# Kernel optimization log

Hardware: AMD Instinct MI355X
Metric: run time of the kernel (lower is better)

The kernel has to match this reference:

```python
import jax, jax.numpy as jnp
import numpy as np

N_HEADS = 16
D_EMBED = 1024
D_HEAD = D_EMBED // N_HEADS
CAUSAL = False


def setup_inputs() -> dict:
    key = jax.random.key(0)
    k1, k2, k3, k4, k5 = jax.random.split(key, 5)
    B, S, D = 4, 2048, D_EMBED
    scale = 1.0 / np.sqrt(D)
    return {
        "x": jax.random.normal(k1, (B, S, D), dtype=jnp.float32),
        "w_in": jax.random.normal(k2, (D, 3 * D), dtype=jnp.float32) * scale,
        "b_in": jax.random.normal(k3, (3 * D,), dtype=jnp.float32) * 0.02,
        "w_out": jax.random.normal(k4, (D, D), dtype=jnp.float32) * scale,
        "b_out": jax.random.normal(k5, (D,), dtype=jnp.float32) * 0.02,
    }


def reference(x, w_in, b_in, w_out, b_out):
    B, S, D = x.shape
    qkv = jnp.einsum("bsd,de->bse", x, w_in) + b_in  # [B,S,3D]
    q, k, v = jnp.split(qkv, 3, axis=-1)
    # split heads -> [B,H,S,Dh]
    def sh(t):
        return t.reshape(B, S, N_HEADS, D_HEAD).transpose(0, 2, 1, 3)
    q, k, v = sh(q), sh(k), sh(v)
    weight = jnp.einsum("bhsd,bhtd->bhst", q, k)  # [B,H,S,S]
    if CAUSAL:
        mask = jnp.triu(jnp.ones((S, S), dtype=bool), k=1)
        weight = jnp.where(mask, -jnp.inf, weight)
    weight = weight / np.sqrt(D_HEAD)
    weight = jax.nn.softmax(weight, axis=-1)
    out = jnp.einsum("bhst,bhtd->bhsd", weight, v)
    out = out.transpose(0, 2, 1, 3).reshape(B, S, D)
    return jnp.einsum("bsd,de->bse", out, w_out) + b_out
```

## Files before the change

### kernel.cpp

```cpp
#include <hip/hip_runtime.h>
#include <hip/hip_bf16.h>

typedef unsigned short u16;
typedef __attribute__((ext_vector_type(8))) short bf16x8;
typedef __attribute__((ext_vector_type(4))) float f32x4;
typedef __attribute__((ext_vector_type(16))) float f32x16;

#define QSCALE 0.180336880f

#define DEV static __device__ __forceinline__

DEV u16 f2bf(float f) {
  union { float f; unsigned u; } v; v.f = f;
  unsigned r = v.u + 0x7fffu + ((v.u >> 16) & 1u);
  return (u16)(r >> 16);
}

DEV unsigned pk2(float a, float b) {
  union { __hip_bfloat162 h; unsigned u; } c;
  c.h = __float22bfloat162_rn(make_float2(a, b));
  return c.u;
}

DEV void gll16(void* lds, const void* g) {
  __builtin_amdgcn_global_load_lds(
      (const __attribute__((address_space(1))) unsigned int*)g,
      (__attribute__((address_space(3))) unsigned int*)lds, 16, 0, 0);
}

__global__ __launch_bounds__(256) void cvt_f32_to_bf16(const float* __restrict__ in,
                                                       u16* __restrict__ out, int n4) {
  int i = blockIdx.x * blockDim.x + threadIdx.x;
  int stride = gridDim.x * blockDim.x;
  for (; i < n4; i += stride) {
    float4 f = ((const float4*)in)[i];
    ushort4 u;
    u.x = f2bf(f.x); u.y = f2bf(f.y); u.z = f2bf(f.z); u.w = f2bf(f.w);
    ((ushort4*)out)[i] = u;
  }
}

__global__ __launch_bounds__(256) void transpose_cvt(const float* __restrict__ W,
                                                     u16* __restrict__ Wt,
                                                     int K, int N, int sn, float sval) {
  __shared__ u16 t[64][65];
  const int k0 = blockIdx.x * 64, n0 = blockIdx.y * 64;
  const int tid = threadIdx.x;
  const int rr = tid >> 4;
  const int cc = (tid & 15) * 4;
  const float scl = (n0 < sn) ? sval : 1.0f;
#pragma unroll
  for (int i = 0; i < 4; ++i) {
    const int row = rr * 4 + i;
    float4 f = *(const float4*)&W[(size_t)(k0 + row) * N + n0 + cc];
    t[row][cc + 0] = f2bf(f.x * scl);
    t[row][cc + 1] = f2bf(f.y * scl);
    t[row][cc + 2] = f2bf(f.z * scl);
    t[row][cc + 3] = f2bf(f.w * scl);
  }
  __syncthreads();
#pragma unroll
  for (int i = 0; i < 4; ++i) {
    const int n = rr * 4 + i;
    ushort4 u;
    u.x = t[cc + 0][n]; u.y = t[cc + 1][n]; u.z = t[cc + 2][n]; u.w = t[cc + 3][n];
    *(ushort4*)&Wt[(size_t)(n0 + n) * K + k0 + cc] = u;
  }
}

__global__ __launch_bounds__(256) void transpose_v(const u16* __restrict__ qkv,
                                                   u16* __restrict__ vT) {
  __shared__ u16 t[64][72];
  const int bh = blockIdx.y;
  const int b = bh >> 4, h = bh & 15;
  const int t0 = blockIdx.x * 64;
  const int tid = threadIdx.x;
  const int row = tid >> 2;
  const int cg = (tid & 3) * 16;
  const size_t src = (size_t)b * 2048 * 3072 + (size_t)(t0 + row) * 3072 + 2048 + h * 64 + cg;
  bf16x8 v0 = *(const bf16x8*)&qkv[src];
  bf16x8 v1 = *(const bf16x8*)&qkv[src + 8];
#pragma unroll
  for (int i = 0; i < 8; ++i) { t[row][cg + i] = (u16)v0[i]; t[row][cg + 8 + i] = (u16)v1[i]; }
  __syncthreads();
  const int d = tid >> 2;
  const int tg = (tid & 3) * 16;
  bf16x8 o0, o1;
#pragma unroll
  for (int i = 0; i < 8; ++i) { o0[i] = (short)t[tg + i][d]; o1[i] = (short)t[tg + 8 + i][d]; }
  u16* dst = &vT[((size_t)bh * 64 + d) * 2048 + t0 + tg];
  *(bf16x8*)dst = o0;
  *(bf16x8*)(dst + 8) = o1;
}

template<bool OUT_BF16>
__global__ __launch_bounds__(256) void gemm_bf16(const u16* __restrict__ A,
                                                 const u16* __restrict__ Bt,
                                                 const float* __restrict__ bias,
                                                 void* __restrict__ Cout,
                                                 int M, int N, int K, int qn,
                                                 u16* __restrict__ vTout, int vn0) {
  __shared__ __align__(16) u16 As[128][64];
  __shared__ __align__(16) u16 Bs[128][64];
  const int tid = threadIdx.x;
  const int wave = tid >> 6, lane = tid & 63;
  const int g = lane >> 4, lr = lane & 15;
  const int bm = blockIdx.x * 128, bn = blockIdx.y * 128;
  const int wm = (wave >> 1) * 64, wn = (wave & 1) * 64;
  f32x4 acc[4][4] = {};
  for (int kt = 0; kt < K; kt += 64) {
    __syncthreads();
#pragma unroll
    for (int j = 0; j < 4; ++j) {
      int chunk = wave * 4 + j;
      int e = chunk * 512 + lane * 8;
      int r = e >> 6, c = e & 63;
      gll16((u16*)As + chunk * 512, &A[(size_t)(bm + r) * K + kt + c]);
      gll16((u16*)Bs + chunk * 512, &Bt[(size_t)(bn + r) * K + kt + c]);
    }
    __syncthreads();
#pragma unroll
    for (int kk = 0; kk < 64; kk += 32) {
      bf16x8 af[4], bfr[4];
#pragma unroll
      for (int m = 0; m < 4; ++m)
        af[m] = *(const bf16x8*)&As[wm + m * 16 + lr][kk + g * 8];
#pragma unroll
      for (int n = 0; n < 4; ++n)
        bfr[n] = *(const bf16x8*)&Bs[wn + n * 16 + lr][kk + g * 8];
#pragma unroll
      for (int m = 0; m < 4; ++m)
#pragma unroll
        for (int n = 0; n < 4; ++n)
          acc[m][n] = __builtin_amdgcn_mfma_f32_16x16x32_bf16(af[m], bfr[n], acc[m][n], 0, 0, 0);
    }
  }
#pragma unroll
  for (int m = 0; m < 4; ++m) {
#pragma unroll
    for (int n = 0; n < 4; ++n) {
      const int col = bn + wn + n * 16 + lr;
      float bv = bias ? bias[col] : 0.f;
      if (col < qn) bv *= QSCALE;
      if (vTout != nullptr && col >= vn0) {
        const int hc = col - vn0;
#pragma unroll
        for (int r = 0; r < 4; ++r) {
          const int row = bm + wm + m * 16 + g * 4 + r;
          const size_t idx = (((size_t)(row >> 11) * 16 + (hc >> 6)) * 64 + (hc & 63)) * 2048
                             + (row & 2047);
          vTout[idx] = f2bf(acc[m][n][r] + bv);
        }
      } else {
#pragma unroll
        for (int r = 0; r < 4; ++r) {
          const int row = bm + wm + m * 16 + g * 4 + r;
          float v = acc[m][n][r] + bv;
          if (OUT_BF16) ((u16*)Cout)[(size_t)row * N + col] = f2bf(v);
          else          ((float*)Cout)[(size_t)row * N + col] = v;
        }
      }
    }
  }
}


#define ATTN_BODY(BUF, PRE)                                                       \
  {                                                                               \
    if (PRE) {                                                                    \
      gll16((u16*)Ks[(BUF) ^ 1] + wave * 512, gk); gk += 32 * 3072;               \
      gll16((u16*)Vs[(BUF) ^ 1] + wave * 512, gv); gv += 32;                      \
    }                                                                             \
    const char* kb = (const char*)Ks[(BUF)];                                      \
    const char* vb = (const char*)Vs[(BUF)];                                      \
    f32x16 s = {};                                                                \
    __builtin_amdgcn_s_setprio(1);                                                \
    _Pragma("unroll")                                                             \
    for (int kk = 0; kk < 4; ++kk) {                                              \
      bf16x8 kf = *(const bf16x8*)(kb + koff[kk]);                                \
      s = __builtin_amdgcn_mfma_f32_32x32x16_bf16(kf, qf[kk], s, 0, 0, 0);        \
    }                                                                             \
    __builtin_amdgcn_s_setprio(0);                                                \
    float t0 = fmaxf(fmaxf(s[0], s[1]), fmaxf(s[2], s[3]));                       \
    float t1 = fmaxf(fmaxf(s[4], s[5]), fmaxf(s[6], s[7]));                       \
    float t2 = fmaxf(fmaxf(s[8], s[9]), fmaxf(s[10], s[11]));                     \
    float t3 = fmaxf(fmaxf(s[12], s[13]), fmaxf(s[14], s[15]));                   \
    float pmax = fmaxf(fmaxf(t0, t1), fmaxf(t2, t3));                             \
    pmax = fmaxf(pmax, __shfl_xor(pmax, 32));                                     \
    if (!__all(pmax <= m + 8.f)) {                                                \
      float mn = fmaxf(m, pmax);                                                  \
      float sc = __builtin_amdgcn_exp2f(m - mn);                                  \
      _Pragma("unroll")                                                           \
      for (int r = 0; r < 16; ++r) {                                              \
        float scr = __shfl(sc, (r & 3) + 8 * (r >> 2) + 4 * hi);                  \
        o0[r] *= scr; o1[r] *= scr;                                               \
      }                                                                           \
      lsum *= sc;                                                                 \
      m = mn;                                                                     \
    }                                                                             \
    float pr[16];                                                                 \
    _Pragma("unroll")                                                             \
    for (int r = 0; r < 16; ++r) pr[r] = __builtin_amdgcn_exp2f(s[r] - m);        \
    lsum += ((pr[0] + pr[1]) + (pr[2] + pr[3])) + ((pr[4] + pr[5]) + (pr[6] + pr[7])) \
          + ((pr[8] + pr[9]) + (pr[10] + pr[11])) + ((pr[12] + pr[13]) + (pr[14] + pr[15])); \
    union { unsigned u[4]; bf16x8 v; } pa0, pa1;                                  \
    {                                                                             \
      unsigned X0 = pk2(pr[0], pr[1]), X1 = pk2(pr[2], pr[3]);                    \
      unsigned Y0 = pk2(pr[4], pr[5]), Y1 = pk2(pr[6], pr[7]);                    \
      asm volatile("v_permlane32_swap_b32 %0, %1" : "+v"(X0), "+v"(Y0));          \
      asm volatile("v_permlane32_swap_b32 %0, %1" : "+v"(X1), "+v"(Y1));          \
      pa0.u[0] = X0; pa0.u[1] = X1; pa0.u[2] = Y0; pa0.u[3] = Y1;                 \
      unsigned Z0 = pk2(pr[8], pr[9]), Z1 = pk2(pr[10], pr[11]);                  \
      unsigned W0 = pk2(pr[12], pr[13]), W1 = pk2(pr[14], pr[15]);                \
      asm volatile("v_permlane32_swap_b32 %0, %1" : "+v"(Z0), "+v"(W0));          \
      asm volatile("v_permlane32_swap_b32 %0, %1" : "+v"(Z1), "+v"(W1));          \
      pa1.u[0] = Z0; pa1.u[1] = Z1; pa1.u[2] = W0; pa1.u[3] = W1;                 \
    }                                                                             \
    __builtin_amdgcn_s_setprio(1);                                                \
    {                                                                             \
      bf16x8 vf00 = *(const bf16x8*)(vb + voff[0][0]);                            \
      bf16x8 vf10 = *(const bf16x8*)(vb + voff[1][0]);                            \
      o0 = __builtin_amdgcn_mfma_f32_32x32x16_bf16(pa0.v, vf00, o0, 0, 0, 0);     \
      o1 = __builtin_amdgcn_mfma_f32_32x32x16_bf16(pa0.v, vf10, o1, 0, 0, 0);     \
      bf16x8 vf01 = *(const bf16x8*)(vb + voff[0][1]);                            \
      bf16x8 vf11 = *(const bf16x8*)(vb + voff[1][1]);                            \
      o0 = __builtin_amdgcn_mfma_f32_32x32x16_bf16(pa1.v, vf01, o0, 0, 0, 0);     \
      o1 = __builtin_amdgcn_mfma_f32_32x32x16_bf16(pa1.v, vf11, o1, 0, 0, 0);     \
    }                                                                             \
    __builtin_amdgcn_s_setprio(0);                                                \
    __syncthreads();                                                              \
  }

__global__ __launch_bounds__(256, 4) void attn_kernel(const u16* __restrict__ qkv,
                                                      const u16* __restrict__ vT,
                                                      u16* __restrict__ out) {
  __shared__ __align__(16) u16 Ks[2][2048];
  __shared__ __align__(16) u16 Vs[2][2048];
  const int tid = threadIdx.x;
  const int wave = tid >> 6, lane = tid & 63;
  const int hi = lane >> 5, l31 = lane & 31;
  const int bh = blockIdx.y;
  const int b = bh >> 4, h = bh & 15;
  const int q0 = blockIdx.x * 128;
  const size_t base = (size_t)b * 2048 * 3072;
  const u16* kg = qkv + base + 1024 + h * 64;
  const u16* vg = vT + (size_t)bh * 64 * 2048;

  const int qrow = q0 + wave * 32 + l31;
  bf16x8 qf[4];
#pragma unroll
  for (int kk = 0; kk < 4; ++kk)
    qf[kk] = *(const bf16x8*)&qkv[base + (size_t)qrow * 3072 + h * 64 + kk * 16 + hi * 8];

  const int rsw = (l31 & 7) << 4;
  int koff[4];
#pragma unroll
  for (int kk = 0; kk < 4; ++kk)
    koff[kk] = l31 * 128 + ((kk * 32 + hi * 16) ^ rsw);
  int voff[2][2];
#pragma unroll
  for (int dt = 0; dt < 2; ++dt)
#pragma unroll
    for (int kp = 0; kp < 2; ++kp)
      voff[dt][kp] = l31 * 128 + ((dt * 64 + kp * 32 + hi * 16) ^ rsw);

  const int a = tid * 16;
  const int row = a >> 7;
  const int cb = (a & 127) ^ ((row & 7) << 4);
  const u16* gk = kg + (size_t)row * 3072 + (cb >> 1);
  const int vd = row + (cb >> 6) * 32;
  const u16* gv = vg + (size_t)vd * 2048 + ((cb & 63) >> 1);

  f32x16 o0 = {}, o1 = {};
  float m = -1e30f, lsum = 0.f;

  gll16((u16*)Ks[0] + wave * 512, gk); gk += 32 * 3072;
  gll16((u16*)Vs[0] + wave * 512, gv); gv += 32;
  __syncthreads();

  for (int it2 = 0; it2 < 32; ++it2) {
    ATTN_BODY(0, 1)
    ATTN_BODY(1, it2 < 31)
  }

  float lt = lsum + __shfl_xor(lsum, 32);
  const size_t orow0 = (size_t)b * 2048 + q0 + wave * 32;
#pragma unroll
  for (int r = 0; r < 16; ++r) {
    const int crow = (r & 3) + 8 * (r >> 2) + 4 * hi;
    const float li = __shfl(lt, crow);
    u16* orow = out + (orow0 + crow) * 1024 + h * 64 + l31;
    orow[0]  = f2bf(o0[r] / li);
    orow[32] = f2bf(o1[r] / li);
  }
}

extern "C" void kernel_launch(void* const* d_in, const int* in_sizes, int n_in,
                              void* d_out, int out_size, void* d_ws, size_t ws_size,
                              hipStream_t stream) {
  (void)in_sizes; (void)n_in; (void)out_size;
  const float* x     = (const float*)d_in[0];
  const float* w_in  = (const float*)d_in[1];
  const float* b_in  = (const float*)d_in[2];
  const float* w_out = (const float*)d_in[3];
  const float* b_out = (const float*)d_in[4];
  float* out = (float*)d_out;

  char* ws = (char*)d_ws;
  u16* Xbf   = (u16*)ws; ws += (size_t)8192 * 1024 * 2;
  u16* WinT  = (u16*)ws; ws += (size_t)3072 * 1024 * 2;
  u16* WoutT = (u16*)ws; ws += (size_t)1024 * 1024 * 2;
  u16* qkv   = (u16*)ws; ws += (size_t)8192 * 3072 * 2;
  u16* attno = (u16*)ws; ws += (size_t)8192 * 1024 * 2;
  u16* vTsep = (u16*)ws;

  const size_t fused_need = 92274688ull + 16777216ull;
  const bool fused = (ws_size >= fused_need);
  u16* vT = fused ? vTsep : Xbf;

  cvt_f32_to_bf16<<<2048, 256, 0, stream>>>(x, Xbf, 8192 * 1024 / 4);
  transpose_cvt<<<dim3(16, 48), 256, 0, stream>>>(w_in, WinT, 1024, 3072, 1024, QSCALE);
  transpose_cvt<<<dim3(16, 16), 256, 0, stream>>>(w_out, WoutT, 1024, 1024, 0, 1.0f);
  if (fused) {
    gemm_bf16<true ><<<dim3(64, 24), 256, 0, stream>>>(Xbf, WinT, b_in, qkv,
                                                       8192, 3072, 1024, 1024, vT, 2048);
  } else {
    gemm_bf16<true ><<<dim3(64, 24), 256, 0, stream>>>(Xbf, WinT, b_in, qkv,
                                                       8192, 3072, 1024, 1024, nullptr, 1 << 30);
    transpose_v<<<dim3(32, 64), 256, 0, stream>>>(qkv, vT);
  }
  attn_kernel<<<dim3(16, 64), 256, 0, stream>>>(qkv, vT, attno);
  gemm_bf16<false><<<dim3(64, 8), 256, 0, stream>>>(attno, WoutT, b_out, out,
                                                    8192, 1024, 1024, 0, nullptr, 1 << 30);
}
```

Baseline: 239.8 us.

## Deepen attention K/V prefetch to four LDS stages with explicit vmcnt waits

The attention kernel now uses a 4-slot LDS ring for K and V tiles and prefetches two tiles ahead. It replaces the trailing __syncthreads with an explicit s_waitcnt vmcnt plus a barrier before each compute step. The LDS layout changes from an XOR-swizzled row layout to a fragment-ordered layout with matching global load addresses. The launch becomes a 1D grid remapped so consecutive blocks cover different heads and batches at the same query tile. The aim is to hide global load latency and improve L2 locality, at the cost of doubling LDS per block, which may lower occupancy, and of relying on manual vmcnt counts being correct.

```diff
diff --git a/kernel.cpp b/kernel.cpp
--- a/kernel.cpp
+++ b/kernel.cpp
@@ -165,12 +165,14 @@
 }
 
 
-#define ATTN_BODY(BUF, PRE)                                                       \
+#define ATTN_BODY(BUF, ISSUE, VM)                                                 \
   {                                                                               \
-    if (PRE) {                                                                    \
-      gll16((u16*)Ks[(BUF) ^ 1] + wave * 512, gk); gk += 32 * 3072;               \
-      gll16((u16*)Vs[(BUF) ^ 1] + wave * 512, gv); gv += 32;                      \
-    }                                                                             \
+    if (ISSUE) {                                                                  \
+      gll16((u16*)Ks[((BUF) + 2) & 3] + wave * 512, gk); gk += 32 * 3072;         \
+      gll16((u16*)Vs[((BUF) + 2) & 3] + wave * 512, gv); gv += 32;                \
+    }                                                                             \
+    asm volatile("s_waitcnt vmcnt(" #VM ")" ::: "memory");                        \
+    __builtin_amdgcn_s_barrier();                                                 \
     const char* kb = (const char*)Ks[(BUF)];                                      \
     const char* vb = (const char*)Vs[(BUF)];                                      \
     f32x16 s = {};                                                                \
@@ -228,20 +230,20 @@
       o1 = __builtin_amdgcn_mfma_f32_32x32x16_bf16(pa1.v, vf11, o1, 0, 0, 0);     \
     }                                                                             \
     __builtin_amdgcn_s_setprio(0);                                                \
-    __syncthreads();                                                              \
   }
 
 __global__ __launch_bounds__(256, 4) void attn_kernel(const u16* __restrict__ qkv,
                                                       const u16* __restrict__ vT,
                                                       u16* __restrict__ out) {
-  __shared__ __align__(16) u16 Ks[2][2048];
-  __shared__ __align__(16) u16 Vs[2][2048];
+  __shared__ __align__(16) u16 Ks[4][2048];
+  __shared__ __align__(16) u16 Vs[4][2048];
   const int tid = threadIdx.x;
   const int wave = tid >> 6, lane = tid & 63;
   const int hi = lane >> 5, l31 = lane & 31;
-  const int bh = blockIdx.y;
+  const int id = blockIdx.x;
+  const int bh = ((id >> 3) & 7) * 8 + (id & 7);
   const int b = bh >> 4, h = bh & 15;
-  const int q0 = blockIdx.x * 128;
+  const int q0 = (id >> 6) * 128;
   const size_t base = (size_t)b * 2048 * 3072;
   const u16* kg = qkv + base + 1024 + h * 64;
   const u16* vg = vT + (size_t)bh * 64 * 2048;
@@ -252,36 +254,38 @@
   for (int kk = 0; kk < 4; ++kk)
     qf[kk] = *(const bf16x8*)&qkv[base + (size_t)qrow * 3072 + h * 64 + kk * 16 + hi * 8];
 
-  const int rsw = (l31 & 7) << 4;
   int koff[4];
 #pragma unroll
   for (int kk = 0; kk < 4; ++kk)
-    koff[kk] = l31 * 128 + ((kk * 32 + hi * 16) ^ rsw);
+    koff[kk] = (kk * 2 + hi) * 512 + l31 * 16;
   int voff[2][2];
 #pragma unroll
   for (int dt = 0; dt < 2; ++dt)
 #pragma unroll
     for (int kp = 0; kp < 2; ++kp)
-      voff[dt][kp] = l31 * 128 + ((dt * 64 + kp * 32 + hi * 16) ^ rsw);
-
-  const int a = tid * 16;
-  const int row = a >> 7;
-  const int cb = (a & 127) ^ ((row & 7) << 4);
-  const u16* gk = kg + (size_t)row * 3072 + (cb >> 1);
-  const int vd = row + (cb >> 6) * 32;
-  const u16* gv = vg + (size_t)vd * 2048 + ((cb & 63) >> 1);
+      voff[dt][kp] = (dt * 4 + kp * 2 + hi) * 512 + l31 * 16;
+
+  const u16* gk = kg + (size_t)l31 * 3072 + wave * 16 + hi * 8;
+  const u16* gv = vg + (size_t)((wave >> 1) * 32 + l31) * 2048 + (wave & 1) * 16 + hi * 8;
 
   f32x16 o0 = {}, o1 = {};
   float m = -1e30f, lsum = 0.f;
 
   gll16((u16*)Ks[0] + wave * 512, gk); gk += 32 * 3072;
   gll16((u16*)Vs[0] + wave * 512, gv); gv += 32;
-  __syncthreads();
-
-  for (int it2 = 0; it2 < 32; ++it2) {
-    ATTN_BODY(0, 1)
-    ATTN_BODY(1, it2 < 31)
-  }
+  gll16((u16*)Ks[1] + wave * 512, gk); gk += 32 * 3072;
+  gll16((u16*)Vs[1] + wave * 512, gv); gv += 32;
+
+  for (int it4 = 0; it4 < 15; ++it4) {
+    ATTN_BODY(0, true, 4)
+    ATTN_BODY(1, true, 4)
+    ATTN_BODY(2, true, 4)
+    ATTN_BODY(3, true, 4)
+  }
+  ATTN_BODY(0, true, 4)
+  ATTN_BODY(1, true, 4)
+  ATTN_BODY(2, false, 2)
+  ATTN_BODY(3, false, 0)
 
   float lt = lsum + __shfl_xor(lsum, 32);
   const size_t orow0 = (size_t)b * 2048 + q0 + wave * 32;
@@ -329,7 +333,7 @@
                                                        8192, 3072, 1024, 1024, nullptr, 1 << 30);
     transpose_v<<<dim3(32, 64), 256, 0, stream>>>(qkv, vT);
   }
-  attn_kernel<<<dim3(16, 64), 256, 0, stream>>>(qkv, vT, attno);
+  attn_kernel<<<1024, 256, 0, stream>>>(qkv, vT, attno);
   gemm_bf16<false><<<dim3(64, 8), 256, 0, stream>>>(attno, WoutT, b_out, out,
                                                     8192, 1024, 1024, 0, nullptr, 1 << 30);
 }
```

After: 239.2 us. No clear change (-0.2%).
